# Kernel optimization log

Measured on AMD Instinct MI355X. Metric: run time of the kernel, lower is better.

## Reference

```python
import jax, jax.numpy as jnp
import numpy as np

N, E, D, R, L = 50000, 600000, 64, 65, 2


def setup_inputs() -> dict:
    key = jax.random.key(0)
    ks = jax.random.split(key, 10)
    x = jax.random.normal(ks[0], (N, D), dtype=jnp.float32)
    edge_index = jax.random.randint(ks[1], (2, E), 0, N, dtype=jnp.int64)
    edge_type = jax.random.randint(ks[2], (E,), 0, R, dtype=jnp.int64)
    s = 1.0 / np.sqrt(D)
    W = jax.random.normal(ks[3], (L, R, D, D), dtype=jnp.float32) * s
    root = jax.random.normal(ks[4], (L, D, D), dtype=jnp.float32) * s
    bias = jax.random.normal(ks[5], (L, D), dtype=jnp.float32) * 0.01
    res_W = jax.random.normal(ks[6], (L, D, D), dtype=jnp.float32) * s
    res_b = jax.random.normal(ks[7], (L, D), dtype=jnp.float32) * 0.01
    return {"x": x, "edge_index": edge_index, "edge_type": edge_type,
            "W": W, "root": root, "bias": bias, "res_W": res_W, "res_b": res_b}


def _rgcn_conv(x, src, dst, edge_type, W_r, W_root, b):
    # PyG RGCNConv (num_bases=None, aggr='mean'):
    #   out_i = x_i @ W_root + b + sum_r mean_{j in N_r(i)} (x_j @ W_r)
    # mean is linear, so aggregate raw features per (node, relation) first,
    # then apply the per-relation transform once per node.
    n, d = x.shape
    r = W_r.shape[0]
    seg = dst * r + edge_type                       # [E]
    msg = x[src]                                    # [E, D] gather
    agg = jax.ops.segment_sum(msg, seg, num_segments=n * r).reshape(n, r, d)
    cnt = jax.ops.segment_sum(jnp.ones((msg.shape[0],), x.dtype), seg,
                              num_segments=n * r).reshape(n, r, 1)
    mean = agg / jnp.maximum(cnt, 1.0)              # [N, R, D]
    out = jnp.einsum('nrd,rdk->nk', mean, W_r)
    return out + x @ W_root + b


def reference(x, edge_index, edge_type, W, root, bias, res_W, res_b):
    src, dst = edge_index[0], edge_index[1]
    h = x
    for l in range(W.shape[0]):
        conv = _rgcn_conv(h, src, dst, edge_type, W[l], root[l], bias[l])
        conv = jax.nn.relu(conv)
        # dropout: identity in eval mode
        res = jax.nn.relu(h @ res_W[l] + res_b[l])
        h = conv + res
    return h
```

## Files before the change

### kernel.cpp

```cpp
#include <hip/hip_runtime.h>


constexpr int NN  = 50000;
constexpr int EE  = 600000;
constexpr int DIM = 64;
constexpr int RR  = 65;
constexpr int MCHUNK = 512;
constexpr int MAXCHUNKS = EE / MCHUNK + RR + 8;
constexpr int SORT_BS = 2048;
constexpr int NSB = (EE + SORT_BS - 1) / SORT_BS;
constexpr int SCAN_BS = 1024;
constexpr int SCAN_NB = (NN + SCAN_BS - 1) / SCAN_BS;
constexpr int XNB = 64;

typedef __attribute__((ext_vector_type(8))) short short8v;
typedef __attribute__((ext_vector_type(4))) float floatx4;

__device__ inline unsigned short f2bf(float f) {
  unsigned int u = __float_as_uint(f);
  return (unsigned short)((u + 0x7fffu + ((u >> 16) & 1u)) >> 16);
}
__device__ inline float bf2f(unsigned short v) {
  return __uint_as_float(((unsigned int)v) << 16);
}


__global__ __launch_bounds__(256) void zero4_k(int4* __restrict__ p, int n4) {
  const int i = blockIdx.x * 256 + threadIdx.x;
  if (i < n4) p[i] = make_int4(0, 0, 0, 0);
}

__global__ __launch_bounds__(512) void hist_k(const int* __restrict__ dst,
                                              const int* __restrict__ et,
                                              unsigned int* __restrict__ cnt32,
                                              int* __restrict__ bhist, int E) {
  __shared__ int lh[RR];
  if (threadIdx.x < RR) lh[threadIdx.x] = 0;
  __syncthreads();
  const int base = blockIdx.x * SORT_BS;
#pragma unroll
  for (int it = 0; it < SORT_BS / 512; ++it) {
    const int e = base + it * 512 + threadIdx.x;
    if (e < E) {
      const int d = dst[e], r = et[e];
      const int c = r * NN + d;
      atomicAdd(&cnt32[c >> 1], 1u << (16 * (c & 1)));
      atomicAdd(&lh[r], 1);
    }
  }
  __syncthreads();
  if (threadIdx.x < RR) bhist[blockIdx.x * RR + threadIdx.x] = lh[threadIdx.x];
}


__global__ __launch_bounds__(1024) void scan1_k(const unsigned short* __restrict__ c16,
                                                int* __restrict__ deg,
                                                int* __restrict__ bsum) {
  __shared__ int s[SCAN_BS];
  const int idx = blockIdx.x * SCAN_BS + threadIdx.x;
  int d = 0;
  if (idx < NN) {
#pragma unroll 13
    for (int r = 0; r < RR; ++r) d += c16[r * NN + idx];
    deg[idx] = d;
  }
  s[threadIdx.x] = d;
  __syncthreads();
  for (int off = SCAN_BS / 2; off > 0; off >>= 1) {
    if (threadIdx.x < off) s[threadIdx.x] += s[threadIdx.x + off];
    __syncthreads();
  }
  if (threadIdx.x == 0) bsum[blockIdx.x] = s[0];
}

__global__ __launch_bounds__(64) void scan2_k(int* __restrict__ bsum) {
  const int t = threadIdx.x;
  int v = (t < SCAN_NB) ? bsum[t] : 0;
  const int orig = v;
  for (int off = 1; off < 64; off <<= 1) {
    const int u = __shfl_up(v, off, 64);
    if (t >= off) v += u;
  }
  if (t < SCAN_NB) bsum[t] = v - orig;
}

__global__ __launch_bounds__(1024) void scan3_k(const int* __restrict__ deg,
                                                const int* __restrict__ bsum,
                                                int* __restrict__ rowptr,
                                                int* __restrict__ poscur) {
  __shared__ int s[SCAN_BS];
  const int t = threadIdx.x;
  const int idx = blockIdx.x * SCAN_BS + t;
  const int v = (idx < NN) ? deg[idx] : 0;
  s[t] = v;
  __syncthreads();
  for (int off = 1; off < SCAN_BS; off <<= 1) {
    const int u = (t >= off) ? s[t - off] : 0;
    __syncthreads();
    s[t] += u;
    __syncthreads();
  }
  const int excl = bsum[blockIdx.x] + s[t] - v;
  if (idx < NN) { rowptr[idx] = excl; poscur[idx] = excl; }
  if (idx == NN - 1) rowptr[NN] = EE;
}


__global__ __launch_bounds__(512) void scan_rel_k(const int* __restrict__ bhist,
                                                  int* __restrict__ boffrel,
                                                  int* __restrict__ total) {
  __shared__ int s[512];
  const int r = blockIdx.x;
  const int t = threadIdx.x;
  const int v = (t < NSB) ? bhist[t * RR + r] : 0;
  s[t] = v;
  __syncthreads();
  for (int off = 1; off < 512; off <<= 1) {
    const int u = (t >= off) ? s[t - off] : 0;
    __syncthreads();
    s[t] += u;
    __syncthreads();
  }
  if (t < NSB) boffrel[t * RR + r] = s[t] - v;
  if (t == 511) total[r] = s[511];
}

__global__ __launch_bounds__(128) void scan_tot_k(const int* __restrict__ total,
                                                  int* __restrict__ tptrg,
                                                  int4* __restrict__ chunkArr,
                                                  int* __restrict__ nchunks) {
  __shared__ int tptr[RR + 1], chbase[RR + 1];
  const int t = threadIdx.x;
  if (t == 0) {
    int run = 0, crun = 0;
    for (int r = 0; r < RR; ++r) {
      tptr[r] = run;    run  += total[r];
      chbase[r] = crun; crun += (total[r] + MCHUNK - 1) / MCHUNK;
    }
    tptr[RR] = run; chbase[RR] = crun;
    *nchunks = crun;
  }
  __syncthreads();
  if (t < RR) {
    tptrg[t] = tptr[t];
    const int tot = total[t];
    const int nc = (tot + MCHUNK - 1) / MCHUNK;
    for (int i = 0; i < nc; ++i) {
      const int beg = tptr[t] + i * MCHUNK;
      chunkArr[chbase[t] + i] = make_int4(beg, min(beg + MCHUNK, tptr[t] + tot), t, 0);
    }
  }
}

__global__ __launch_bounds__(512) void scatter_k(const int* __restrict__ src,
                                                 const int* __restrict__ dst,
                                                 const int* __restrict__ et,
                                                 const unsigned short* __restrict__ c16,
                                                 const int* __restrict__ boffrel,
                                                 const int* __restrict__ tptrg,
                                                 int* __restrict__ poscur,
                                                 int* __restrict__ osrc,
                                                 int* __restrict__ opos,
                                                 float* __restrict__ oscale, int E) {
  __shared__ int cur[RR];
  if (threadIdx.x < RR)
    cur[threadIdx.x] = tptrg[threadIdx.x] + boffrel[blockIdx.x * RR + threadIdx.x];
  __syncthreads();
  const int base = blockIdx.x * SORT_BS;
#pragma unroll
  for (int it = 0; it < SORT_BS / 512; ++it) {
    const int e = base + it * 512 + threadIdx.x;
    if (e < E) {
      const int s = src[e], d = dst[e], r = et[e];
      const int q = atomicAdd(&cur[r], 1);
      const int p = atomicAdd(&poscur[d], 1);
      osrc[q] = s;
      opos[q] = p;
      oscale[q] = 1.0f / (float)c16[r * NN + d];
    }
  }
}


__global__ __launch_bounds__(256) void cvtw_k(const float* __restrict__ W,
                                              unsigned short* __restrict__ WT) {
  const int tid = blockIdx.x * 256 + threadIdx.x;
  const int total4 = 2 * RR * DIM * DIM / 4;
  if (tid >= total4) return;
  const int base = tid * 4;
  const int mat = base >> 12;
  const int rem = base & 4095;
  const int k = rem >> 6, c0 = rem & 63;
  const float4 v = *reinterpret_cast<const float4*>(W + base);
  unsigned short* o = WT + (size_t)mat * 4096;
  o[(c0 + 0) * 64 + k] = f2bf(v.x);
  o[(c0 + 1) * 64 + k] = f2bf(v.y);
  o[(c0 + 2) * 64 + k] = f2bf(v.z);
  o[(c0 + 3) * 64 + k] = f2bf(v.w);
}


__global__ __launch_bounds__(512) void msgm_k(const unsigned short* __restrict__ hbf,
                                              const int* __restrict__ osrc,
                                              const int* __restrict__ opos,
                                              const float* __restrict__ oscale,
                                              const unsigned short* __restrict__ WT,
                                              const int4* __restrict__ chunkArr,
                                              const int* __restrict__ nchunks,
                                              unsigned short* __restrict__ m) {
  const int ci = blockIdx.x;
  if (ci >= *nchunks) return;
  const int4 c = chunkArr[ci];
  const int beg = c.x, end = c.y, rel = c.z;

  __shared__ unsigned short Wl[DIM][72];
  {
    const float4* s4 = reinterpret_cast<const float4*>(WT + (size_t)rel * 4096);
    const int seg = threadIdx.x;
    const int row = seg >> 3, s8 = seg & 7;
    *reinterpret_cast<float4*>(&Wl[row][s8 * 8]) = s4[seg];
  }
  __syncthreads();

  const int w  = threadIdx.x >> 6;
  const int l  = threadIdx.x & 63;
  const int lr = l & 15, lq = l >> 4;

  const int ebase = beg + w * 64;
  if (ebase >= end) return;

  short8v a[4][2];
#pragma unroll
  for (int ct = 0; ct < 4; ++ct)
#pragma unroll
    for (int kk = 0; kk < 2; ++kk)
      a[ct][kk] = *reinterpret_cast<const short8v*>(&Wl[ct * 16 + lr][kk * 32 + lq * 8]);

  short8v b[4][2];
  int eidx[4];
#pragma unroll
  for (int et = 0; et < 4; ++et) {
    eidx[et] = ebase + et * 16 + lr;
    const int e = min(eidx[et], end - 1);
    const int s = osrc[e];
    const unsigned short* hp = hbf + (size_t)s * DIM;
    b[et][0] = *reinterpret_cast<const short8v*>(hp + lq * 8);
    b[et][1] = *reinterpret_cast<const short8v*>(hp + 32 + lq * 8);
  }

  floatx4 acc[4][4];
#pragma unroll
  for (int ct = 0; ct < 4; ++ct)
#pragma unroll
    for (int et = 0; et < 4; ++et)
      acc[ct][et] = (floatx4){0.f, 0.f, 0.f, 0.f};

#pragma unroll
  for (int kk = 0; kk < 2; ++kk)
#pragma unroll
    for (int ct = 0; ct < 4; ++ct)
#pragma unroll
      for (int et = 0; et < 4; ++et)
        acc[ct][et] = __builtin_amdgcn_mfma_f32_16x16x32_bf16(a[ct][kk], b[et][kk],
                                                              acc[ct][et], 0, 0, 0);

#pragma unroll
  for (int et = 0; et < 4; ++et) {
    const int e = eidx[et];
    if (e < end) {
      const float sc = oscale[e];
      unsigned short* op = m + (size_t)opos[e] * DIM;
#pragma unroll
      for (int ct = 0; ct < 4; ++ct) {
        ushort4 o;
        o.x = f2bf(acc[ct][et][0] * sc);
        o.y = f2bf(acc[ct][et][1] * sc);
        o.z = f2bf(acc[ct][et][2] * sc);
        o.w = f2bf(acc[ct][et][3] * sc);
        *reinterpret_cast<ushort4*>(op + ct * 16 + lq * 4) = o;
      }
    }
  }
}

__global__ __launch_bounds__(256) void xform_k(const float* __restrict__ h,
                                               const float* __restrict__ root,
                                               const float* __restrict__ bias,
                                               const float* __restrict__ rw,
                                               const float* __restrict__ rb,
                                               float* __restrict__ rt,
                                               float* __restrict__ rs,
                                               unsigned short* __restrict__ hbf, int N) {
  __shared__ float Wl0[DIM * DIM];
  __shared__ float Wl1[DIM * DIM];
  __shared__ float xs[XNB][68];
#pragma unroll
  for (int i = 0; i < 4; ++i) {
    reinterpret_cast<float4*>(Wl0)[threadIdx.x + i * 256] =
        reinterpret_cast<const float4*>(root)[threadIdx.x + i * 256];
    reinterpret_cast<float4*>(Wl1)[threadIdx.x + i * 256] =
        reinterpret_cast<const float4*>(rw)[threadIdx.x + i * 256];
  }

  const int g = threadIdx.x >> 4, li = threadIdx.x & 15;
  const int base = blockIdx.x * XNB;
#pragma unroll
  for (int r = 0; r < 4; ++r) {
    const int n = base + g * 4 + r;
    float4 v = make_float4(0.f, 0.f, 0.f, 0.f);
    if (n < N) v = *reinterpret_cast<const float4*>(h + (size_t)n * DIM + li * 4);
    *reinterpret_cast<float4*>(&xs[g * 4 + r][li * 4]) = v;
  }
  __syncthreads();

  if (hbf != nullptr) {
#pragma unroll
    for (int r = 0; r < 4; ++r) {
      const int n = base + g * 4 + r;
      if (n < N) {
        const float4 v = *reinterpret_cast<const float4*>(&xs[g * 4 + r][li * 4]);
        ushort4 o;
        o.x = f2bf(v.x); o.y = f2bf(v.y); o.z = f2bf(v.z); o.w = f2bf(v.w);
        *reinterpret_cast<ushort4*>(hbf + (size_t)n * DIM + li * 4) = o;
      }
    }
  }

  float aR[4][4], aS[4][4];
#pragma unroll
  for (int r = 0; r < 4; ++r)
#pragma unroll
    for (int q = 0; q < 4; ++q) { aR[r][q] = 0.f; aS[r][q] = 0.f; }

#pragma unroll 4
  for (int k = 0; k < DIM; ++k) {
    const float4 wr = *reinterpret_cast<const float4*>(&Wl0[k * DIM + li * 4]);
    const float4 wv = *reinterpret_cast<const float4*>(&Wl1[k * DIM + li * 4]);
#pragma unroll
    for (int r = 0; r < 4; ++r) {
      const float xv = xs[g * 4 + r][k];
      aR[r][0] += xv * wr.x; aR[r][1] += xv * wr.y; aR[r][2] += xv * wr.z; aR[r][3] += xv * wr.w;
      aS[r][0] += xv * wv.x; aS[r][1] += xv * wv.y; aS[r][2] += xv * wv.z; aS[r][3] += xv * wv.w;
    }
  }

  const float4 bv = reinterpret_cast<const float4*>(bias)[li];
  const float4 cv = reinterpret_cast<const float4*>(rb)[li];
#pragma unroll
  for (int r = 0; r < 4; ++r) {
    const int n = base + g * 4 + r;
    if (n < N) {
      *reinterpret_cast<float4*>(rt + (size_t)n * DIM + li * 4) =
          make_float4(aR[r][0] + bv.x, aR[r][1] + bv.y, aR[r][2] + bv.z, aR[r][3] + bv.w);
      *reinterpret_cast<float4*>(rs + (size_t)n * DIM + li * 4) =
          make_float4(fmaxf(aS[r][0] + cv.x, 0.f), fmaxf(aS[r][1] + cv.y, 0.f),
                      fmaxf(aS[r][2] + cv.z, 0.f), fmaxf(aS[r][3] + cv.w, 0.f));
    }
  }
}

__global__ __launch_bounds__(256) void gather2_k(const unsigned short* __restrict__ m,
                                                 const int* __restrict__ rowptr,
                                                 const float* __restrict__ rt,
                                                 const float* __restrict__ rs,
                                                 float* __restrict__ hout, int N) {
  const int g = threadIdx.x >> 4, li = threadIdx.x & 15;
  const int n = blockIdx.x * 16 + g;
  if (n >= N) return;

  float a0 = 0.f, a1 = 0.f, a2 = 0.f, a3 = 0.f;
  const int jb = rowptr[n], je = rowptr[n + 1];
  int j = jb;
  for (; j + 8 <= je; j += 8) {
    ushort4 v[8];
#pragma unroll
    for (int u = 0; u < 8; ++u)
      v[u] = *reinterpret_cast<const ushort4*>(m + (size_t)(j + u) * DIM + li * 4);
#pragma unroll
    for (int u = 0; u < 8; ++u) {
      a0 += bf2f(v[u].x); a1 += bf2f(v[u].y); a2 += bf2f(v[u].z); a3 += bf2f(v[u].w);
    }
  }
  for (; j + 4 <= je; j += 4) {
    ushort4 v[4];
#pragma unroll
    for (int u = 0; u < 4; ++u)
      v[u] = *reinterpret_cast<const ushort4*>(m + (size_t)(j + u) * DIM + li * 4);
#pragma unroll
    for (int u = 0; u < 4; ++u) {
      a0 += bf2f(v[u].x); a1 += bf2f(v[u].y); a2 += bf2f(v[u].z); a3 += bf2f(v[u].w);
    }
  }
  for (; j < je; ++j) {
    const ushort4 v = *reinterpret_cast<const ushort4*>(m + (size_t)j * DIM + li * 4);
    a0 += bf2f(v.x); a1 += bf2f(v.y); a2 += bf2f(v.z); a3 += bf2f(v.w);
  }

  const float4 t = *reinterpret_cast<const float4*>(rt + (size_t)n * DIM + li * 4);
  const float4 s = *reinterpret_cast<const float4*>(rs + (size_t)n * DIM + li * 4);
  *reinterpret_cast<float4*>(hout + (size_t)n * DIM + li * 4) =
      make_float4(fmaxf(a0 + t.x, 0.f) + s.x, fmaxf(a1 + t.y, 0.f) + s.y,
                  fmaxf(a2 + t.z, 0.f) + s.z, fmaxf(a3 + t.w, 0.f) + s.w);
}


__global__ __launch_bounds__(256) void count_k(const int* __restrict__ dst,
                                               const int* __restrict__ et,
                                               int* __restrict__ cnt, int E) {
  int e = blockIdx.x * 256 + threadIdx.x;
  if (e < E) atomicAdd(&cnt[dst[e] * RR + et[e]], 1);
}

__global__ __launch_bounds__(256) void edge_k(const float* __restrict__ h,
                                              const int* __restrict__ src,
                                              const int* __restrict__ dst,
                                              const int* __restrict__ et,
                                              const float* __restrict__ W,
                                              const int* __restrict__ cnt,
                                              float* __restrict__ accum, int E) {
  __shared__ float xs[16][68];
  const int g = threadIdx.x >> 4, li = threadIdx.x & 15;
  const int e = blockIdx.x * 16 + g;
  if (e >= E) return;
  const int s = src[e], d = dst[e], t = et[e];
  *reinterpret_cast<float4*>(&xs[g][li * 4]) =
      *reinterpret_cast<const float4*>(h + (size_t)s * DIM + li * 4);
  const float* Wt = W + (size_t)t * (DIM * DIM) + li * 4;
  float a0 = 0.f, a1 = 0.f, a2 = 0.f, a3 = 0.f;
#pragma unroll 8
  for (int k = 0; k < DIM; ++k) {
    const float xd = xs[g][k];
    const float4 w = *reinterpret_cast<const float4*>(Wt + k * DIM);
    a0 += xd * w.x; a1 += xd * w.y; a2 += xd * w.z; a3 += xd * w.w;
  }
  const float sc = 1.0f / (float)cnt[d * RR + t];
  float* o = accum + (size_t)d * DIM + li * 4;
  unsafeAtomicAdd(o + 0, a0 * sc);
  unsafeAtomicAdd(o + 1, a1 * sc);
  unsafeAtomicAdd(o + 2, a2 * sc);
  unsafeAtomicAdd(o + 3, a3 * sc);
}

__global__ __launch_bounds__(256) void node_k(const float* __restrict__ h,
                                              const float* __restrict__ root,
                                              const float* __restrict__ bias,
                                              const float* __restrict__ rw,
                                              const float* __restrict__ rb,
                                              float* __restrict__ io, int N) {
  __shared__ float xs[16][68];
  const int g = threadIdx.x >> 4, li = threadIdx.x & 15;
  const int n = blockIdx.x * 16 + g;
  if (n >= N) return;
  *reinterpret_cast<float4*>(&xs[g][li * 4]) =
      *reinterpret_cast<const float4*>(h + (size_t)n * DIM + li * 4);
  float r0 = 0.f, r1 = 0.f, r2 = 0.f, r3 = 0.f;
  float s0 = 0.f, s1 = 0.f, s2 = 0.f, s3 = 0.f;
#pragma unroll 8
  for (int k = 0; k < DIM; ++k) {
    const float hd = xs[g][k];
    const float4 w = *reinterpret_cast<const float4*>(root + k * DIM + li * 4);
    const float4 v = *reinterpret_cast<const float4*>(rw + k * DIM + li * 4);
    r0 += hd * w.x; r1 += hd * w.y; r2 += hd * w.z; r3 += hd * w.w;
    s0 += hd * v.x; s1 += hd * v.y; s2 += hd * v.z; s3 += hd * v.w;
  }
  float* o = io + (size_t)n * DIM + li * 4;
  const float4 acc = *reinterpret_cast<const float4*>(o);
  const float4 b = *reinterpret_cast<const float4*>(bias + li * 4);
  const float4 c = *reinterpret_cast<const float4*>(rb + li * 4);
  float o0 = fmaxf(acc.x + r0 + b.x, 0.f) + fmaxf(s0 + c.x, 0.f);
  float o1 = fmaxf(acc.y + r1 + b.y, 0.f) + fmaxf(s1 + c.y, 0.f);
  float o2 = fmaxf(acc.z + r2 + b.z, 0.f) + fmaxf(s2 + c.z, 0.f);
  float o3 = fmaxf(acc.w + r3 + b.w, 0.f) + fmaxf(s3 + c.w, 0.f);
  *reinterpret_cast<float4*>(o) = make_float4(o0, o1, o2, o3);
}


extern "C" void kernel_launch(void* const* d_in, const int* in_sizes, int n_in,
                              void* d_out, int out_size, void* d_ws, size_t ws_size,
                              hipStream_t stream) {
  const float* x    = (const float*)d_in[0];
  const int*   ei   = (const int*)d_in[1];
  const int*   et   = (const int*)d_in[2];
  const float* W    = (const float*)d_in[3];
  const float* root = (const float*)d_in[4];
  const float* bias = (const float*)d_in[5];
  const float* resW = (const float*)d_in[6];
  const float* resb = (const float*)d_in[7];
  float* out = (float*)d_out;

  const int* src = ei;
  const int* dstp = ei + EE;

  char* ws = (char*)d_ws;
  size_t off = 0;
  auto take = [&](size_t bytes) -> void* {
    void* p = ws + off;
    off = (off + bytes + 255) & ~(size_t)255;
    return p;
  };
  unsigned short* m = (unsigned short*)take((size_t)EE * DIM * sizeof(unsigned short));
  float* h1      = (float*)take((size_t)NN * DIM * sizeof(float));
  int* deg       = (int*)take((size_t)NN * sizeof(int));
  int* rowptr    = (int*)take((size_t)(NN + 1) * sizeof(int));
  int* poscur    = (int*)take((size_t)NN * sizeof(int));
  int* bhist     = (int*)take((size_t)NSB * RR * sizeof(int));
  int* boffrel   = (int*)take((size_t)NSB * RR * sizeof(int));
  int* total     = (int*)take((size_t)RR * sizeof(int));
  int* tptrg     = (int*)take((size_t)RR * sizeof(int));
  int* bsum      = (int*)take((size_t)SCAN_NB * sizeof(int));
  int* osrc      = (int*)take((size_t)EE * sizeof(int));
  int* opos      = (int*)take((size_t)EE * sizeof(int));
  float* oscale  = (float*)take((size_t)EE * sizeof(float));
  int4* chunkArr = (int4*)take((size_t)MAXCHUNKS * sizeof(int4));
  int* nchunks   = (int*)take(256);
  float* rt      = (float*)take((size_t)NN * DIM * sizeof(float));
  float* rs      = (float*)take((size_t)NN * DIM * sizeof(float));
  unsigned short* hbf = (unsigned short*)take((size_t)NN * DIM * sizeof(unsigned short));
  unsigned short* wbt = (unsigned short*)take((size_t)2 * RR * DIM * DIM * sizeof(unsigned short));
  const size_t main_off = off;
  unsigned int* cnt32 = (unsigned int*)m;
  const unsigned short* c16 = (const unsigned short*)m;

  if (main_off <= ws_size) {
    zero4_k<<<(NN * RR * 2 / 16 + 255) / 256, 256, 0, stream>>>((int4*)cnt32, NN * RR * 2 / 16);
    hist_k<<<NSB, 512, 0, stream>>>(dstp, et, cnt32, bhist, EE);
    scan1_k<<<SCAN_NB, 1024, 0, stream>>>(c16, deg, bsum);
    scan2_k<<<1, 64, 0, stream>>>(bsum);
    scan3_k<<<SCAN_NB, 1024, 0, stream>>>(deg, bsum, rowptr, poscur);
    scan_rel_k<<<RR, 512, 0, stream>>>(bhist, boffrel, total);
    scan_tot_k<<<1, 128, 0, stream>>>(total, tptrg, chunkArr, nchunks);
    scatter_k<<<NSB, 512, 0, stream>>>(src, dstp, et, c16, boffrel, tptrg, poscur,
                                       osrc, opos, oscale, EE);
    cvtw_k<<<(2 * RR * DIM * DIM / 4 + 255) / 256, 256, 0, stream>>>(W, wbt);

    const int XG = (NN + XNB - 1) / XNB;
    xform_k<<<XG, 256, 0, stream>>>(x, root, bias, resW, resb, rt, rs, hbf, NN);
    msgm_k<<<MAXCHUNKS, 512, 0, stream>>>(hbf, osrc, opos, oscale, wbt, chunkArr, nchunks, m);
    gather2_k<<<(NN + 15) / 16, 256, 0, stream>>>(m, rowptr, rt, rs, h1, NN);
    xform_k<<<XG, 256, 0, stream>>>(h1, root + DIM * DIM, bias + DIM,
                                    resW + DIM * DIM, resb + DIM, rt, rs, hbf, NN);
    msgm_k<<<MAXCHUNKS, 512, 0, stream>>>(hbf, osrc, opos, oscale,
                                          wbt + (size_t)RR * DIM * DIM, chunkArr, nchunks, m);
    gather2_k<<<(NN + 15) / 16, 256, 0, stream>>>(m, rowptr, rt, rs, out, NN);
  } else {
    int* fcnt = (int*)ws;
    float* fh1 = (float*)(ws + (size_t)NN * RR * sizeof(int));
    hipMemsetAsync(fcnt, 0, (size_t)NN * RR * sizeof(int), stream);
    hipMemsetAsync(fh1, 0, (size_t)NN * DIM * sizeof(float), stream);
    hipMemsetAsync(out, 0, (size_t)NN * DIM * sizeof(float), stream);
    count_k<<<(EE + 255) / 256, 256, 0, stream>>>(dstp, et, fcnt, EE);
    edge_k<<<(EE + 15) / 16, 256, 0, stream>>>(x, src, dstp, et, W, fcnt, fh1, EE);
    node_k<<<(NN + 15) / 16, 256, 0, stream>>>(x, root, bias, resW, resb, fh1, NN);
    edge_k<<<(EE + 15) / 16, 256, 0, stream>>>(fh1, src, dstp, et,
                                               W + (size_t)RR * DIM * DIM, fcnt, out, EE);
    node_k<<<(NN + 15) / 16, 256, 0, stream>>>(fh1, root + DIM * DIM, bias + DIM,
                                               resW + DIM * DIM, resb + DIM, out, NN);
  }
}
```

Baseline: 251.8 us.

## Merge setup kernels, store intermediates in bf16, halve message chunk size

```diff
diff --git a/kernel.cpp b/kernel.cpp
--- a/kernel.cpp
+++ b/kernel.cpp
@@ -5,8 +5,8 @@
 constexpr int EE  = 600000;
 constexpr int DIM = 64;
 constexpr int RR  = 65;
-constexpr int MCHUNK = 512;
-constexpr int MAXCHUNKS = EE / MCHUNK + RR + 8;
+constexpr int CHUNK = 256;
+constexpr int MAXCHUNKS = EE / CHUNK + RR + 8;
 constexpr int SORT_BS = 2048;
 constexpr int NSB = (EE + SORT_BS - 1) / SORT_BS;
 constexpr int SCAN_BS = 1024;
@@ -25,9 +25,44 @@
 }
 
 
-__global__ __launch_bounds__(256) void zero4_k(int4* __restrict__ p, int n4) {
-  const int i = blockIdx.x * 256 + threadIdx.x;
-  if (i < n4) p[i] = make_int4(0, 0, 0, 0);
+constexpr int ZN4 = NN * RR * 2 / 16;
+constexpr int ZB  = (ZN4 + 255) / 256;
+constexpr int CW4 = 2 * RR * DIM * DIM / 4;
+constexpr int CB  = (CW4 + 255) / 256;
+constexpr int HB  = (NN * DIM / 8 + 255) / 256;
+
+__global__ __launch_bounds__(256) void setup_k(int4* __restrict__ zp,
+                                               const float* __restrict__ W,
+                                               unsigned short* __restrict__ WT,
+                                               const float* __restrict__ x,
+                                               unsigned short* __restrict__ hbf) {
+  const int b = blockIdx.x;
+  if (b < ZB) {
+    const int i = b * 256 + threadIdx.x;
+    if (i < ZN4) zp[i] = make_int4(0, 0, 0, 0);
+  } else if (b < ZB + CB) {
+    const int tid = (b - ZB) * 256 + threadIdx.x;
+    if (tid >= CW4) return;
+    const int base = tid * 4;
+    const int mat = base >> 12, rem = base & 4095;
+    const int k = rem >> 6, c0 = rem & 63;
+    const float4 v = *reinterpret_cast<const float4*>(W + base);
+    unsigned short* o = WT + (size_t)mat * 4096;
+    o[(c0 + 0) * 64 + k] = f2bf(v.x);
+    o[(c0 + 1) * 64 + k] = f2bf(v.y);
+    o[(c0 + 2) * 64 + k] = f2bf(v.z);
+    o[(c0 + 3) * 64 + k] = f2bf(v.w);
+  } else {
+    const int tid = (b - ZB - CB) * 256 + threadIdx.x;
+    if (tid * 8 >= NN * DIM) return;
+    const float4 v0 = reinterpret_cast<const float4*>(x)[tid * 2];
+    const float4 v1 = reinterpret_cast<const float4*>(x)[tid * 2 + 1];
+    ushort4 a, c;
+    a.x = f2bf(v0.x); a.y = f2bf(v0.y); a.z = f2bf(v0.z); a.w = f2bf(v0.w);
+    c.x = f2bf(v1.x); c.y = f2bf(v1.y); c.z = f2bf(v1.z); c.w = f2bf(v1.w);
+    reinterpret_cast<ushort4*>(hbf)[tid * 2] = a;
+    reinterpret_cast<ushort4*>(hbf)[tid * 2 + 1] = c;
+  }
 }
 
 __global__ __launch_bounds__(512) void hist_k(const int* __restrict__ dst,
@@ -53,35 +88,84 @@
 }
 
 
-__global__ __launch_bounds__(1024) void scan1_k(const unsigned short* __restrict__ c16,
+__global__ __launch_bounds__(1024) void scanA_k(const unsigned short* __restrict__ c16,
                                                 int* __restrict__ deg,
-                                                int* __restrict__ bsum) {
+                                                int* __restrict__ bsum,
+                                                const int* __restrict__ bhist,
+                                                int* __restrict__ boffrel,
+                                                int* __restrict__ total) {
   __shared__ int s[SCAN_BS];
-  const int idx = blockIdx.x * SCAN_BS + threadIdx.x;
-  int d = 0;
-  if (idx < NN) {
+  const int t = threadIdx.x;
+  if (blockIdx.x < SCAN_NB) {
+    const int idx = blockIdx.x * SCAN_BS + t;
+    int d = 0;
+    if (idx < NN) {
 #pragma unroll 13
-    for (int r = 0; r < RR; ++r) d += c16[r * NN + idx];
-    deg[idx] = d;
-  }
-  s[threadIdx.x] = d;
-  __syncthreads();
-  for (int off = SCAN_BS / 2; off > 0; off >>= 1) {
-    if (threadIdx.x < off) s[threadIdx.x] += s[threadIdx.x + off];
+      for (int r = 0; r < RR; ++r) d += c16[r * NN + idx];
+      deg[idx] = d;
+    }
+    s[t] = d;
     __syncthreads();
-  }
-  if (threadIdx.x == 0) bsum[blockIdx.x] = s[0];
-}
-
-__global__ __launch_bounds__(64) void scan2_k(int* __restrict__ bsum) {
+    for (int off = SCAN_BS / 2; off > 0; off >>= 1) {
+      if (t < off) s[t] += s[t + off];
+      __syncthreads();
+    }
+    if (t == 0) bsum[blockIdx.x] = s[0];
+  } else {
+    const int r = blockIdx.x - SCAN_NB;
+    const int v = (t < NSB) ? bhist[t * RR + r] : 0;
+    s[t] = v;
+    __syncthreads();
+    for (int off = 1; off < SCAN_BS; off <<= 1) {
+      const int u = (t >= off) ? s[t - off] : 0;
+      __syncthreads();
+      s[t] += u;
+      __syncthreads();
+    }
+    if (t < NSB) boffrel[t * RR + r] = s[t] - v;
+    if (t == SCAN_BS - 1) total[r] = s[SCAN_BS - 1];
+  }
+}
+
+
+__global__ __launch_bounds__(128) void scanB_k(int* __restrict__ bsum,
+                                               const int* __restrict__ total,
+                                               int* __restrict__ tptrg,
+                                               int4* __restrict__ chunkArr,
+                                               int* __restrict__ nchunks) {
   const int t = threadIdx.x;
-  int v = (t < SCAN_NB) ? bsum[t] : 0;
-  const int orig = v;
-  for (int off = 1; off < 64; off <<= 1) {
-    const int u = __shfl_up(v, off, 64);
-    if (t >= off) v += u;
-  }
-  if (t < SCAN_NB) bsum[t] = v - orig;
+  if (blockIdx.x == 0) {
+    if (t < 64) {
+      int v = (t < SCAN_NB) ? bsum[t] : 0;
+      const int orig = v;
+      for (int off = 1; off < 64; off <<= 1) {
+        const int u = __shfl_up(v, off, 64);
+        if (t >= off) v += u;
+      }
+      if (t < SCAN_NB) bsum[t] = v - orig;
+    }
+  } else {
+    __shared__ int tptr[RR + 1], chbase[RR + 1];
+    if (t == 0) {
+      int run = 0, crun = 0;
+      for (int r = 0; r < RR; ++r) {
+        tptr[r] = run;    run  += total[r];
+        chbase[r] = crun; crun += (total[r] + CHUNK - 1) / CHUNK;
+      }
+      tptr[RR] = run; chbase[RR] = crun;
+      *nchunks = crun;
+    }
+    __syncthreads();
+    if (t < RR) {
+      tptrg[t] = tptr[t];
+      const int tot = total[t];
+      const int nc = (tot + CHUNK - 1) / CHUNK;
+      for (int i = 0; i < nc; ++i) {
+        const int beg = tptr[t] + i * CHUNK;
+        chunkArr[chbase[t] + i] = make_int4(beg, min(beg + CHUNK, tptr[t] + tot), t, 0);
+      }
+    }
+  }
 }
 
 __global__ __launch_bounds__(1024) void scan3_k(const int* __restrict__ deg,
@@ -105,53 +189,6 @@
   if (idx == NN - 1) rowptr[NN] = EE;
 }
 
-
-__global__ __launch_bounds__(512) void scan_rel_k(const int* __restrict__ bhist,
-                                                  int* __restrict__ boffrel,
-                                                  int* __restrict__ total) {
-  __shared__ int s[512];
-  const int r = blockIdx.x;
-  const int t = threadIdx.x;
-  const int v = (t < NSB) ? bhist[t * RR + r] : 0;
-  s[t] = v;
-  __syncthreads();
-  for (int off = 1; off < 512; off <<= 1) {
-    const int u = (t >= off) ? s[t - off] : 0;
-    __syncthreads();
-    s[t] += u;
-    __syncthreads();
-  }
-  if (t < NSB) boffrel[t * RR + r] = s[t] - v;
-  if (t == 511) total[r] = s[511];
-}
-
-__global__ __launch_bounds__(128) void scan_tot_k(const int* __restrict__ total,
-                                                  int* __restrict__ tptrg,
-                                                  int4* __restrict__ chunkArr,
-                                                  int* __restrict__ nchunks) {
-  __shared__ int tptr[RR + 1], chbase[RR + 1];
-  const int t = threadIdx.x;
-  if (t == 0) {
-    int run = 0, crun = 0;
-    for (int r = 0; r < RR; ++r) {
-      tptr[r] = run;    run  += total[r];
-      chbase[r] = crun; crun += (total[r] + MCHUNK - 1) / MCHUNK;
-    }
-    tptr[RR] = run; chbase[RR] = crun;
-    *nchunks = crun;
-  }
-  __syncthreads();
-  if (t < RR) {
-    tptrg[t] = tptr[t];
-    const int tot = total[t];
-    const int nc = (tot + MCHUNK - 1) / MCHUNK;
-    for (int i = 0; i < nc; ++i) {
-      const int beg = tptr[t] + i * MCHUNK;
-      chunkArr[chbase[t] + i] = make_int4(beg, min(beg + MCHUNK, tptr[t] + tot), t, 0);
-    }
-  }
-}
-
 __global__ __launch_bounds__(512) void scatter_k(const int* __restrict__ src,
                                                  const int* __restrict__ dst,
                                                  const int* __restrict__ et,
@@ -182,25 +219,7 @@
 }
 
 
-__global__ __launch_bounds__(256) void cvtw_k(const float* __restrict__ W,
-                                              unsigned short* __restrict__ WT) {
-  const int tid = blockIdx.x * 256 + threadIdx.x;
-  const int total4 = 2 * RR * DIM * DIM / 4;
-  if (tid >= total4) return;
-  const int base = tid * 4;
-  const int mat = base >> 12;
-  const int rem = base & 4095;
-  const int k = rem >> 6, c0 = rem & 63;
-  const float4 v = *reinterpret_cast<const float4*>(W + base);
-  unsigned short* o = WT + (size_t)mat * 4096;
-  o[(c0 + 0) * 64 + k] = f2bf(v.x);
-  o[(c0 + 1) * 64 + k] = f2bf(v.y);
-  o[(c0 + 2) * 64 + k] = f2bf(v.z);
-  o[(c0 + 3) * 64 + k] = f2bf(v.w);
-}
-
-
-__global__ __launch_bounds__(512) void msgm_k(const unsigned short* __restrict__ hbf,
+__global__ __launch_bounds__(256) void msgm_k(const unsigned short* __restrict__ hbf,
                                               const int* __restrict__ osrc,
                                               const int* __restrict__ opos,
                                               const float* __restrict__ oscale,
@@ -216,9 +235,12 @@
   __shared__ unsigned short Wl[DIM][72];
   {
     const float4* s4 = reinterpret_cast<const float4*>(WT + (size_t)rel * 4096);
-    const int seg = threadIdx.x;
-    const int row = seg >> 3, s8 = seg & 7;
-    *reinterpret_cast<float4*>(&Wl[row][s8 * 8]) = s4[seg];
+#pragma unroll
+    for (int it = 0; it < 2; ++it) {
+      const int seg = threadIdx.x + it * 256;
+      const int row = seg >> 3, s8 = seg & 7;
+      *reinterpret_cast<float4*>(&Wl[row][s8 * 8]) = s4[seg];
+    }
   }
   __syncthreads();
 
@@ -283,14 +305,14 @@
   }
 }
 
-__global__ __launch_bounds__(256) void xform_k(const float* __restrict__ h,
+template<bool F32SRC>
+__global__ __launch_bounds__(256) void xform_k(const void* __restrict__ hsrc,
                                                const float* __restrict__ root,
                                                const float* __restrict__ bias,
                                                const float* __restrict__ rw,
                                                const float* __restrict__ rb,
-                                               float* __restrict__ rt,
-                                               float* __restrict__ rs,
-                                               unsigned short* __restrict__ hbf, int N) {
+                                               unsigned short* __restrict__ rt16,
+                                               unsigned short* __restrict__ rs16, int N) {
   __shared__ float Wl0[DIM * DIM];
   __shared__ float Wl1[DIM * DIM];
   __shared__ float xs[XNB][68];
@@ -308,23 +330,18 @@
   for (int r = 0; r < 4; ++r) {
     const int n = base + g * 4 + r;
     float4 v = make_float4(0.f, 0.f, 0.f, 0.f);
-    if (n < N) v = *reinterpret_cast<const float4*>(h + (size_t)n * DIM + li * 4);
+    if (n < N) {
+      if (F32SRC) {
+        v = *reinterpret_cast<const float4*>((const float*)hsrc + (size_t)n * DIM + li * 4);
+      } else {
+        const ushort4 u = *reinterpret_cast<const ushort4*>(
+            (const unsigned short*)hsrc + (size_t)n * DIM + li * 4);
+        v = make_float4(bf2f(u.x), bf2f(u.y), bf2f(u.z), bf2f(u.w));
+      }
+    }
     *reinterpret_cast<float4*>(&xs[g * 4 + r][li * 4]) = v;
   }
   __syncthreads();
-
-  if (hbf != nullptr) {
-#pragma unroll
-    for (int r = 0; r < 4; ++r) {
-      const int n = base + g * 4 + r;
-      if (n < N) {
-        const float4 v = *reinterpret_cast<const float4*>(&xs[g * 4 + r][li * 4]);
-        ushort4 o;
-        o.x = f2bf(v.x); o.y = f2bf(v.y); o.z = f2bf(v.z); o.w = f2bf(v.w);
-        *reinterpret_cast<ushort4*>(hbf + (size_t)n * DIM + li * 4) = o;
-      }
-    }
-  }
 
   float aR[4][4], aS[4][4];
 #pragma unroll
@@ -350,20 +367,23 @@
   for (int r = 0; r < 4; ++r) {
     const int n = base + g * 4 + r;
     if (n < N) {
-      *reinterpret_cast<float4*>(rt + (size_t)n * DIM + li * 4) =
-          make_float4(aR[r][0] + bv.x, aR[r][1] + bv.y, aR[r][2] + bv.z, aR[r][3] + bv.w);
-      *reinterpret_cast<float4*>(rs + (size_t)n * DIM + li * 4) =
-          make_float4(fmaxf(aS[r][0] + cv.x, 0.f), fmaxf(aS[r][1] + cv.y, 0.f),
-                      fmaxf(aS[r][2] + cv.z, 0.f), fmaxf(aS[r][3] + cv.w, 0.f));
-    }
-  }
-}
-
+      ushort4 t, s;
+      t.x = f2bf(aR[r][0] + bv.x); t.y = f2bf(aR[r][1] + bv.y);
+      t.z = f2bf(aR[r][2] + bv.z); t.w = f2bf(aR[r][3] + bv.w);
+      s.x = f2bf(fmaxf(aS[r][0] + cv.x, 0.f)); s.y = f2bf(fmaxf(aS[r][1] + cv.y, 0.f));
+      s.z = f2bf(fmaxf(aS[r][2] + cv.z, 0.f)); s.w = f2bf(fmaxf(aS[r][3] + cv.w, 0.f));
+      *reinterpret_cast<ushort4*>(rt16 + (size_t)n * DIM + li * 4) = t;
+      *reinterpret_cast<ushort4*>(rs16 + (size_t)n * DIM + li * 4) = s;
+    }
+  }
+}
+
+template<bool OUT_BF16>
 __global__ __launch_bounds__(256) void gather2_k(const unsigned short* __restrict__ m,
                                                  const int* __restrict__ rowptr,
-                                                 const float* __restrict__ rt,
-                                                 const float* __restrict__ rs,
-                                                 float* __restrict__ hout, int N) {
+                                                 const unsigned short* __restrict__ rt16,
+                                                 const unsigned short* __restrict__ rs16,
+                                                 void* __restrict__ hout, int N) {
   const int g = threadIdx.x >> 4, li = threadIdx.x & 15;
   const int n = blockIdx.x * 16 + g;
   if (n >= N) return;
@@ -396,11 +416,20 @@
     a0 += bf2f(v.x); a1 += bf2f(v.y); a2 += bf2f(v.z); a3 += bf2f(v.w);
   }
 
-  const float4 t = *reinterpret_cast<const float4*>(rt + (size_t)n * DIM + li * 4);
-  const float4 s = *reinterpret_cast<const float4*>(rs + (size_t)n * DIM + li * 4);
-  *reinterpret_cast<float4*>(hout + (size_t)n * DIM + li * 4) =
-      make_float4(fmaxf(a0 + t.x, 0.f) + s.x, fmaxf(a1 + t.y, 0.f) + s.y,
-                  fmaxf(a2 + t.z, 0.f) + s.z, fmaxf(a3 + t.w, 0.f) + s.w);
+  const ushort4 tu = *reinterpret_cast<const ushort4*>(rt16 + (size_t)n * DIM + li * 4);
+  const ushort4 su = *reinterpret_cast<const ushort4*>(rs16 + (size_t)n * DIM + li * 4);
+  const float o0 = fmaxf(a0 + bf2f(tu.x), 0.f) + bf2f(su.x);
+  const float o1 = fmaxf(a1 + bf2f(tu.y), 0.f) + bf2f(su.y);
+  const float o2 = fmaxf(a2 + bf2f(tu.z), 0.f) + bf2f(su.z);
+  const float o3 = fmaxf(a3 + bf2f(tu.w), 0.f) + bf2f(su.w);
+  if (OUT_BF16) {
+    ushort4 o;
+    o.x = f2bf(o0); o.y = f2bf(o1); o.z = f2bf(o2); o.w = f2bf(o3);
+    *reinterpret_cast<ushort4*>((unsigned short*)hout + (size_t)n * DIM + li * 4) = o;
+  } else {
+    *reinterpret_cast<float4*>((float*)hout + (size_t)n * DIM + li * 4) =
+        make_float4(o0, o1, o2, o3);
+  }
 }
 
 
@@ -499,7 +528,6 @@
     return p;
   };
   unsigned short* m = (unsigned short*)take((size_t)EE * DIM * sizeof(unsigned short));
-  float* h1      = (float*)take((size_t)NN * DIM * sizeof(float));
   int* deg       = (int*)take((size_t)NN * sizeof(int));
   int* rowptr    = (int*)take((size_t)(NN + 1) * sizeof(int));
   int* poscur    = (int*)take((size_t)NN * sizeof(int));
@@ -513,35 +541,32 @@
   float* oscale  = (float*)take((size_t)EE * sizeof(float));
   int4* chunkArr = (int4*)take((size_t)MAXCHUNKS * sizeof(int4));
   int* nchunks   = (int*)take(256);
-  float* rt      = (float*)take((size_t)NN * DIM * sizeof(float));
-  float* rs      = (float*)take((size_t)NN * DIM * sizeof(float));
-  unsigned short* hbf = (unsigned short*)take((size_t)NN * DIM * sizeof(unsigned short));
-  unsigned short* wbt = (unsigned short*)take((size_t)2 * RR * DIM * DIM * sizeof(unsigned short));
+  unsigned short* rt16 = (unsigned short*)take((size_t)NN * DIM * sizeof(unsigned short));
+  unsigned short* rs16 = (unsigned short*)take((size_t)NN * DIM * sizeof(unsigned short));
+  unsigned short* hbf  = (unsigned short*)take((size_t)NN * DIM * sizeof(unsigned short));
+  unsigned short* wbt  = (unsigned short*)take((size_t)2 * RR * DIM * DIM * sizeof(unsigned short));
   const size_t main_off = off;
   unsigned int* cnt32 = (unsigned int*)m;
   const unsigned short* c16 = (const unsigned short*)m;
 
   if (main_off <= ws_size) {
-    zero4_k<<<(NN * RR * 2 / 16 + 255) / 256, 256, 0, stream>>>((int4*)cnt32, NN * RR * 2 / 16);
+    setup_k<<<ZB + CB + HB, 256, 0, stream>>>((int4*)cnt32, W, wbt, x, hbf);
     hist_k<<<NSB, 512, 0, stream>>>(dstp, et, cnt32, bhist, EE);
-    scan1_k<<<SCAN_NB, 1024, 0, stream>>>(c16, deg, bsum);
-    scan2_k<<<1, 64, 0, stream>>>(bsum);
+    scanA_k<<<SCAN_NB + RR, 1024, 0, stream>>>(c16, deg, bsum, bhist, boffrel, total);
+    scanB_k<<<2, 128, 0, stream>>>(bsum, total, tptrg, chunkArr, nchunks);
     scan3_k<<<SCAN_NB, 1024, 0, stream>>>(deg, bsum, rowptr, poscur);
-    scan_rel_k<<<RR, 512, 0, stream>>>(bhist, boffrel, total);
-    scan_tot_k<<<1, 128, 0, stream>>>(total, tptrg, chunkArr, nchunks);
     scatter_k<<<NSB, 512, 0, stream>>>(src, dstp, et, c16, boffrel, tptrg, poscur,
                                        osrc, opos, oscale, EE);
-    cvtw_k<<<(2 * RR * DIM * DIM / 4 + 255) / 256, 256, 0, stream>>>(W, wbt);
 
     const int XG = (NN + XNB - 1) / XNB;
-    xform_k<<<XG, 256, 0, stream>>>(x, root, bias, resW, resb, rt, rs, hbf, NN);
-    msgm_k<<<MAXCHUNKS, 512, 0, stream>>>(hbf, osrc, opos, oscale, wbt, chunkArr, nchunks, m);
-    gather2_k<<<(NN + 15) / 16, 256, 0, stream>>>(m, rowptr, rt, rs, h1, NN);
-    xform_k<<<XG, 256, 0, stream>>>(h1, root + DIM * DIM, bias + DIM,
-                                    resW + DIM * DIM, resb + DIM, rt, rs, hbf, NN);
-    msgm_k<<<MAXCHUNKS, 512, 0, stream>>>(hbf, osrc, opos, oscale,
+    xform_k<true><<<XG, 256, 0, stream>>>(x, root, bias, resW, resb, rt16, rs16, NN);
+    msgm_k<<<MAXCHUNKS, 256, 0, stream>>>(hbf, osrc, opos, oscale, wbt, chunkArr, nchunks, m);
+    gather2_k<true><<<(NN + 15) / 16, 256, 0, stream>>>(m, rowptr, rt16, rs16, hbf, NN);
+    xform_k<false><<<XG, 256, 0, stream>>>(hbf, root + DIM * DIM, bias + DIM,
+                                           resW + DIM * DIM, resb + DIM, rt16, rs16, NN);
+    msgm_k<<<MAXCHUNKS, 256, 0, stream>>>(hbf, osrc, opos, oscale,
                                           wbt + (size_t)RR * DIM * DIM, chunkArr, nchunks, m);
-    gather2_k<<<(NN + 15) / 16, 256, 0, stream>>>(m, rowptr, rt, rs, out, NN);
+    gather2_k<false><<<(NN + 15) / 16, 256, 0, stream>>>(m, rowptr, rt16, rs16, out, NN);
   } else {
     int* fcnt = (int*)ws;
     float* fh1 = (float*)(ws + (size_t)NN * RR * sizeof(int));
```

New measurement: 230.2 us. 1.09x faster.
